# Performance work log

Hardware: AMD Instinct MI355X
Metric: run time of the kernel (lower is better)

## Reference

```python
import jax, jax.numpy as jnp
import numpy as np

# Network topology constants (topological order: inputs, L hidden layers, outputs)
N_IN = 512
H = 1024      # hidden nodes per layer
L = 8         # hidden layers
N_OUT = 256
DEG = 64      # enabled incoming connections per non-input node
B = 1024      # batch of input vectors

LAYER_SIZES = [H] * L + [N_OUT]
E_TOTAL = sum(n * DEG for n in LAYER_SIZES)  # 540672


def setup_inputs() -> dict:
    key = jax.random.key(0)
    k_in, k_w = jax.random.split(key)
    inputs = jax.random.normal(k_in, (B, N_IN), dtype=jnp.float32)
    # scale weights ~1/sqrt(DEG) so sigmoid pre-activations are well-conditioned
    weights = jax.random.normal(k_w, (E_TOTAL,), dtype=jnp.float32) / np.sqrt(DEG)
    # src indices: for each layer, incoming edges may come from ANY earlier node
    rng = np.random.default_rng(0)
    src_chunks = []
    n_before = N_IN
    for n in LAYER_SIZES:
        src_chunks.append(rng.integers(0, n_before, size=n * DEG))
        n_before += n
    src_idx = jnp.asarray(np.concatenate(src_chunks), dtype=jnp.int32)
    return {"inputs": inputs, "weights": weights, "src_idx": src_idx}


def reference(inputs, weights, src_idx):
    # outs: [B, n_nodes_evaluated_so_far], grown layer by layer (topological order)
    outs = inputs
    off = 0
    for n in LAYER_SIZES:
        e = n * DEG
        s = src_idx[off:off + e]            # [e] gather indices into earlier nodes
        w = weights[off:off + e]            # [e]
        gathered = outs[:, s] * w           # [B, e] irregular gather + scale
        z = gathered.reshape(-1, n, DEG).sum(-1)  # per-node sum over DEG in-edges
        outs = jnp.concatenate([outs, jax.nn.sigmoid(z)], axis=1)
        off += e
    return outs[:, -N_OUT:]  # [B, N_OUT] outputs of 'output' nodes
```

## Files before the change

### kernel.cpp

```cpp
#include <hip/hip_runtime.h>
#include <math.h>


#define N_IN    512
#define NLAYER  9
#define DEG     64
#define BATCH   1024
#define BPB     4
#define THREADS 1024
#define TOTAL_N 8960
#define N_OUT   256
#define NGROUP  132

union H4 { uint2 u; _Float16 h[4]; };
union H2 { unsigned u; _Float16 h[2]; };
union HS { _Float16 h; unsigned short s; };

__global__ __launch_bounds__(64)
void neat_prep(const float* __restrict__ wts,
               const int*   __restrict__ sidx,
               uint4*       __restrict__ rec)
{
    __shared__ int            lidx[64 * 65];
    __shared__ unsigned short lw  [64 * 65];
    __shared__ int            sbin[64 * 17];
    __shared__ unsigned short srec[64 * 16 * 8];

    const int t     = threadIdx.x;
    const int g     = blockIdx.x;
    const int ebase = g << 12;

    for (int k = 0; k < 64; ++k) {
        const int j = ebase + (k << 6) + t;
        lidx[k * 65 + t] = sidx[j];
        HS w; w.h = (_Float16)wts[j];
        lw[k * 65 + t] = w.s;
    }
    __syncthreads();

    #pragma unroll
    for (int b = 0; b < 16; ++b) sbin[t * 17 + b] = 0;
    for (int e = 0; e < DEG; ++e) sbin[t * 17 + (lidx[t * 65 + e] & 15)]++;

    int run = 0;
    #pragma unroll
    for (int b = 0; b < 16; ++b) { int c = sbin[t*17+b]; sbin[t*17+b] = run; run += c; }

    const int sigma = ((t & 15) << 2) | (t >> 4);
    for (int e = 0; e < DEG; ++e) {
        const int idx  = lidx[t * 65 + e];
        const int p    = sbin[t * 17 + (idx & 15)]++;
        const int slot = (p - sigma) & 63;
        const int q = slot >> 2, gg = slot & 3;
        srec[(t * 16 + q) * 8 + gg]     = (unsigned short)idx;
        srec[(t * 16 + q) * 8 + 4 + gg] = lw[t * 65 + e];
    }

    const uint4* sr = reinterpret_cast<const uint4*>(srec);
    for (int q = 0; q < 16; ++q)
        rec[(g << 10) + (q << 6) + t] = sr[t * 16 + q];
}

__global__ __launch_bounds__(THREADS, 4)
void neat_fwd(const float* __restrict__ in,
              const uint4* __restrict__ rec,
              float*       __restrict__ out)
{
    __shared__ _Float16 act[TOTAL_N * BPB];

    const int tid   = threadIdx.x;
    const int bbase = blockIdx.x * BPB;

    {
        const float* src = in + bbase * N_IN;
        for (int t = tid; t < BPB * N_IN; t += THREADS) {
            int j = t >> 9;
            int i = t & (N_IN - 1);
            act[i * BPB + j] = (_Float16)src[t];
        }
    }
    __syncthreads();

    int recBase = 0;
    int nb      = N_IN;
    #pragma unroll 1
    for (int layer = 0; layer < NLAYER; ++layer) {
        const int n = (layer < NLAYER - 1) ? 1024 : N_OUT;
        if (tid < n) {
            const int neuron = tid;
            const uint4* rp = rec + recBase + ((neuron >> 6) << 10) + (neuron & 63);

            uint4 r[16];
            #pragma unroll
            for (int q = 0; q < 16; ++q) r[q] = rp[q << 6];

            float4 acc = make_float4(0.f, 0.f, 0.f, 0.f);
            #pragma unroll
            for (int q = 0; q < 16; ++q) {
                const uint4 r4 = r[q];
                H4 g0, g1, g2, g3;
                g0.u = *reinterpret_cast<const uint2*>(act + ((r4.x & 0xffffu) << 2));
                g1.u = *reinterpret_cast<const uint2*>(act + ((r4.x >> 16) << 2));
                g2.u = *reinterpret_cast<const uint2*>(act + ((r4.y & 0xffffu) << 2));
                g3.u = *reinterpret_cast<const uint2*>(act + ((r4.y >> 16) << 2));
                H2 wz, ww; wz.u = r4.z; ww.u = r4.w;
                acc.x += (float)g0.h[0] * (float)wz.h[0];
                acc.y += (float)g0.h[1] * (float)wz.h[0];
                acc.z += (float)g0.h[2] * (float)wz.h[0];
                acc.w += (float)g0.h[3] * (float)wz.h[0];
                acc.x += (float)g1.h[0] * (float)wz.h[1];
                acc.y += (float)g1.h[1] * (float)wz.h[1];
                acc.z += (float)g1.h[2] * (float)wz.h[1];
                acc.w += (float)g1.h[3] * (float)wz.h[1];
                acc.x += (float)g2.h[0] * (float)ww.h[0];
                acc.y += (float)g2.h[1] * (float)ww.h[0];
                acc.z += (float)g2.h[2] * (float)ww.h[0];
                acc.w += (float)g2.h[3] * (float)ww.h[0];
                acc.x += (float)g3.h[0] * (float)ww.h[1];
                acc.y += (float)g3.h[1] * (float)ww.h[1];
                acc.z += (float)g3.h[2] * (float)ww.h[1];
                acc.w += (float)g3.h[3] * (float)ww.h[1];
            }

            float4 sg;
            sg.x = 1.f / (1.f + __expf(-acc.x));
            sg.y = 1.f / (1.f + __expf(-acc.y));
            sg.z = 1.f / (1.f + __expf(-acc.z));
            sg.w = 1.f / (1.f + __expf(-acc.w));

            if (layer < NLAYER - 1) {
                H4 p;
                p.h[0] = (_Float16)sg.x; p.h[1] = (_Float16)sg.y;
                p.h[2] = (_Float16)sg.z; p.h[3] = (_Float16)sg.w;
                *reinterpret_cast<uint2*>(act + ((nb + neuron) << 2)) = p.u;
            } else {
                float* op = out + neuron;
                op[(bbase + 0) * N_OUT] = sg.x;
                op[(bbase + 1) * N_OUT] = sg.y;
                op[(bbase + 2) * N_OUT] = sg.z;
                op[(bbase + 3) * N_OUT] = sg.w;
            }
        }
        __syncthreads();
        recBase += n << 4;
        nb      += n;
    }
}

extern "C" void kernel_launch(void* const* d_in, const int* in_sizes, int n_in,
                              void* d_out, int out_size, void* d_ws, size_t ws_size,
                              hipStream_t stream)
{
    const float* in  = (const float*)d_in[0];
    const float* wts = (const float*)d_in[1];
    const int*   sx  = (const int*)d_in[2];
    float*       out = (float*)d_out;
    uint4*       rec = (uint4*)d_ws;

    neat_prep<<<NGROUP, 64, 0, stream>>>(wts, sx, rec);
    neat_fwd<<<BATCH / BPB, THREADS, 0, stream>>>(in, rec, out);
}
```

Before: 55.23 us.

## Rewrite prep kernel bucketing with wave ballots across 256 threads

The preprocessing kernel now uses 256 threads per block. Each wave handles 16 neurons, with one lane per edge, and computes each edge's bucket position using 16 ballot/popcount steps instead of a per-thread serial histogram over shared memory. The shared record buffer is padded to a stride of 17 to reduce bank conflicts on the transposed write-out. This aims to cut the serial latency of the prep kernel, which runs on only 132 small blocks, at the cost of extra ballot instructions per edge.

```diff
diff --git a/kernel.cpp b/kernel.cpp
--- a/kernel.cpp
+++ b/kernel.cpp
@@ -16,49 +16,48 @@
 union H2 { unsigned u; _Float16 h[2]; };
 union HS { _Float16 h; unsigned short s; };
 
-__global__ __launch_bounds__(64)
+__global__ __launch_bounds__(256)
 void neat_prep(const float* __restrict__ wts,
                const int*   __restrict__ sidx,
                uint4*       __restrict__ rec)
 {
-    __shared__ int            lidx[64 * 65];
-    __shared__ unsigned short lw  [64 * 65];
-    __shared__ int            sbin[64 * 17];
-    __shared__ unsigned short srec[64 * 16 * 8];
+    __shared__ unsigned short srec[64 * 17 * 8];
 
-    const int t     = threadIdx.x;
-    const int g     = blockIdx.x;
-    const int ebase = g << 12;
+    const int tid  = threadIdx.x;
+    const int g    = blockIdx.x;
+    const int wave = tid >> 6;
+    const int lane = tid & 63;
+    const unsigned long long lt = (1ull << lane) - 1ull;
 
-    for (int k = 0; k < 64; ++k) {
-        const int j = ebase + (k << 6) + t;
-        lidx[k * 65 + t] = sidx[j];
+    #pragma unroll 2
+    for (int k = 0; k < 16; ++k) {
+        const int l = (wave << 4) + k;
+        const int j = (g << 12) + (l << 6) + lane;
+        const int idx = sidx[j];
         HS w; w.h = (_Float16)wts[j];
-        lw[k * 65 + t] = w.s;
+
+        const int c = idx & 15;
+        int start = 0, rank = 0;
+        #pragma unroll
+        for (int cc = 0; cc < 16; ++cc) {
+            const unsigned long long m = __ballot(c == cc);
+            if (cc < c)       start += (int)__popcll(m);
+            else if (cc == c) rank   = (int)__popcll(m & lt);
+        }
+
+        const int sigma = ((l & 15) << 2) | (l >> 4);
+        const int slot  = ((start + rank) - sigma) & 63;
+        const int q = slot >> 2, gg = slot & 3;
+        srec[((l * 17 + q) << 3) + gg]     = (unsigned short)idx;
+        srec[((l * 17 + q) << 3) + 4 + gg] = w.s;
     }
     __syncthreads();
 
-    #pragma unroll
-    for (int b = 0; b < 16; ++b) sbin[t * 17 + b] = 0;
-    for (int e = 0; e < DEG; ++e) sbin[t * 17 + (lidx[t * 65 + e] & 15)]++;
-
-    int run = 0;
-    #pragma unroll
-    for (int b = 0; b < 16; ++b) { int c = sbin[t*17+b]; sbin[t*17+b] = run; run += c; }
-
-    const int sigma = ((t & 15) << 2) | (t >> 4);
-    for (int e = 0; e < DEG; ++e) {
-        const int idx  = lidx[t * 65 + e];
-        const int p    = sbin[t * 17 + (idx & 15)]++;
-        const int slot = (p - sigma) & 63;
-        const int q = slot >> 2, gg = slot & 3;
-        srec[(t * 16 + q) * 8 + gg]     = (unsigned short)idx;
-        srec[(t * 16 + q) * 8 + 4 + gg] = lw[t * 65 + e];
+    const uint4* sr = reinterpret_cast<const uint4*>(srec);
+    for (int r = tid; r < 1024; r += 256) {
+        const int q = r >> 6, l = r & 63;
+        rec[(g << 10) + r] = sr[l * 17 + q];
     }
-
-    const uint4* sr = reinterpret_cast<const uint4*>(srec);
-    for (int q = 0; q < 16; ++q)
-        rec[(g << 10) + (q << 6) + t] = sr[t * 16 + q];
 }
 
 __global__ __launch_bounds__(THREADS, 4)
@@ -157,6 +156,6 @@
     float*       out = (float*)d_out;
     uint4*       rec = (uint4*)d_ws;
 
-    neat_prep<<<NGROUP, 64, 0, stream>>>(wts, sx, rec);
+    neat_prep<<<NGROUP, 256, 0, stream>>>(wts, sx, rec);
     neat_fwd<<<BATCH / BPB, THREADS, 0, stream>>>(in, rec, out);
 }
```

Result: no change. 55.33 us (+0.2%).
